# Performance work log

Measured on AMD Instinct MI355X. Metric: run time of the kernel, lower is better.

The kernel has to match this reference:

```python
import jax, jax.numpy as jnp
import numpy as np
from jax import lax

B, T, D, H = 64, 512, 256, 256


def lstm_scan(x_seq, Wih, Whh, bih, bhh):
    """Run an LSTMCell over time. x_seq: [B, T, D] -> hidden states [B, T, H].
    Gate order i, f, g, o (torch LSTMCell convention)."""
    Bv, Tv, _ = x_seq.shape
    Hv = Whh.shape[1]
    # Precompute input projection once: [B, T, 4H]
    x_proj = jnp.einsum('btd,gd->btg', x_seq, Wih) + bih + bhh

    def step(carry, xp):
        h, c = carry
        gates = xp + h @ Whh.T  # [B, 4H]
        i, f, g, o = jnp.split(gates, 4, axis=-1)
        c = jax.nn.sigmoid(f) * c + jax.nn.sigmoid(i) * jnp.tanh(g)
        h = jax.nn.sigmoid(o) * jnp.tanh(c)
        return (h, c), h

    init = (jnp.zeros((Bv, Hv), x_seq.dtype), jnp.zeros((Bv, Hv), x_seq.dtype))
    _, hs = lax.scan(step, init, jnp.swapaxes(x_proj, 0, 1))  # [T, B, H]
    return jnp.swapaxes(hs, 0, 1)


def bilstm(x, input_length, Wih_f, Whh_f, bih_f, bhh_f, Wih_b, Whh_b, bih_b, bhh_b):
    Bv, L, _ = x.shape
    t = jnp.arange(L)
    lens = input_length.astype(jnp.int32)
    # Inversed input exactly as _get_inversed_input: for t < len -> x[len-1-t],
    # for t >= len -> x[L-1-(t-len)] (unused tail, faithful to original).
    inv_idx = L - 1 - ((L - lens[:, None] + t[None, :]) % L)  # [B, L]
    xn = jnp.take_along_axis(x, inv_idx[:, :, None], axis=1)

    fwd_h = lstm_scan(x, Wih_f, Whh_f, bih_f, bhh_f)   # [B, L, H]
    bwd_h = lstm_scan(xn, Wih_b, Whh_b, bih_b, bhh_b)  # [B, L, H]

    # Re-reverse the backward states over valid region; zero-pad beyond length.
    mask = t[None, :] < lens[:, None]                   # [B, L]
    bwd_idx = jnp.clip(lens[:, None] - 1 - t[None, :], 0, L - 1)
    bwd_g = jnp.take_along_axis(bwd_h, bwd_idx[:, :, None], axis=1)
    out = jnp.concatenate([fwd_h, bwd_g], axis=-1)      # [B, L, 2H]
    return jnp.where(mask[:, :, None], out, jnp.zeros((), out.dtype))


def setup_inputs() -> dict:
    key = jax.random.key(0)
    ks = jax.random.split(key, 10)
    s = 0.05
    return {
        'x': jax.random.normal(ks[0], (B, T, D), jnp.float32),
        'input_length': jax.random.randint(ks[1], (B,), 1, T + 1, jnp.int32),
        'Wih_f': jax.random.normal(ks[2], (4 * H, D), jnp.float32) * s,
        'Whh_f': jax.random.normal(ks[3], (4 * H, H), jnp.float32) * s,
        'bih_f': jax.random.normal(ks[4], (4 * H,), jnp.float32) * s,
        'bhh_f': jax.random.normal(ks[5], (4 * H,), jnp.float32) * s,
        'Wih_b': jax.random.normal(ks[6], (4 * H, D), jnp.float32) * s,
        'Whh_b': jax.random.normal(ks[7], (4 * H, H), jnp.float32) * s,
        'bih_b': jax.random.normal(ks[8], (4 * H,), jnp.float32) * s,
        'bhh_b': jax.random.normal(ks[9], (4 * H,), jnp.float32) * s,
    }


def reference(x, input_length, Wih_f, Whh_f, bih_f, bhh_f, Wih_b, Whh_b, bih_b, bhh_b):
    return bilstm(x, input_length, Wih_f, Whh_f, bih_f, bhh_f, Wih_b, Whh_b, bih_b, bhh_b)
```

## Files before the change

### kernel.cpp

```cpp
#include <hip/hip_runtime.h>
#include <cstdio>


typedef unsigned short ushort_t;
typedef __attribute__((ext_vector_type(8))) short short8;
typedef __attribute__((ext_vector_type(4))) float f32x4;

__device__ __forceinline__ ushort_t f2bf(float f) {
    union { float f; unsigned u; } v; v.f = f;
    unsigned r = v.u + 0x7fffu + ((v.u >> 16) & 1u);
    return (ushort_t)(r >> 16);
}
__device__ __forceinline__ float bf2f(ushort_t h) {
    union { unsigned u; float f; } v; v.u = ((unsigned)h) << 16;
    return v.f;
}

__device__ __forceinline__ float fexp2(float x) {
#if __has_builtin(__builtin_amdgcn_exp2f)
    return __builtin_amdgcn_exp2f(x);
#else
    return exp2f(x);
#endif
}
__device__ __forceinline__ float frcp(float x) {
#if __has_builtin(__builtin_amdgcn_rcpf)
    return __builtin_amdgcn_rcpf(x);
#else
    return 1.0f / x;
#endif
}
__device__ __forceinline__ float fsig(float x) {
    return frcp(1.0f + fexp2(-1.44269504089f * x));
}
__device__ __forceinline__ float ftanh(float x) {
    float e = fexp2(2.88539008178f * x);
    return 1.0f - 2.0f * frcp(e + 1.0f);
}

__device__ __forceinline__ int dot4(int a, int b, int c) {
#if __has_builtin(__builtin_amdgcn_sdot4)
    return __builtin_amdgcn_sdot4(a, b, c, false);
#else
    int r = c;
    r += ((a << 24) >> 24) * ((b << 24) >> 24);
    r += ((a << 16) >> 24) * ((b << 16) >> 24);
    r += ((a << 8) >> 24) * ((b << 8) >> 24);
    r += (a >> 24) * (b >> 24);
    return r;
#endif
}

__device__ __forceinline__ void lds_barrier() {
    asm volatile("s_waitcnt lgkmcnt(0)\n\ts_barrier" ::: "memory");
}

__global__ __launch_bounds__(256) void k_f2bf(const float* __restrict__ in,
                                              ushort_t* __restrict__ out, int n) {
    int i = (blockIdx.x * 256 + threadIdx.x) * 4;
    if (i + 3 < n) {
        float4 v = *(const float4*)&in[i];
        ushort4 o;
        o.x = f2bf(v.x); o.y = f2bf(v.y); o.z = f2bf(v.z); o.w = f2bf(v.w);
        *(ushort4*)&out[i] = o;
    }
}

__global__ __launch_bounds__(256) void k_wih(const float* __restrict__ wihf,
                                             const float* __restrict__ wihb,
                                             ushort_t* __restrict__ dst) {
    int d = blockIdx.y;
    int n = blockIdx.x * 4 + (threadIdx.x >> 6);
    int l = threadIdx.x & 63;
    const float* src = (d ? wihb : wihf) + (size_t)n * 256;
    float4 v = *(const float4*)&src[l * 4];
    int np = (n & 255) * 4 + (n >> 8);
    ushort4 o;
    o.x = f2bf(v.x); o.y = f2bf(v.y); o.z = f2bf(v.z); o.w = f2bf(v.w);
    *(ushort4*)&dst[((size_t)d * 1024 + np) * 256 + l * 4] = o;
}

__global__ __launch_bounds__(256) void k_bias(const float* __restrict__ bihf,
                                              const float* __restrict__ bhhf,
                                              const float* __restrict__ bihb,
                                              const float* __restrict__ bhhb,
                                              float* __restrict__ bv) {
    int i = blockIdx.x * 256 + threadIdx.x;
    int d = i >> 10, n = i & 1023;
    float s = d ? (bihb[n] + bhhb[n]) : (bihf[n] + bhhf[n]);
    bv[d * 1024 + (n & 255) * 4 + (n >> 8)] = s;
}

__global__ __launch_bounds__(256) void k_quant(const float* __restrict__ whhf,
                                               const float* __restrict__ whhb,
                                               int* __restrict__ wq4,
                                               float* __restrict__ fscale4) {
    int rowg = blockIdx.x * 4 + (threadIdx.x >> 6);
    int l = threadIdx.x & 63;
    int d = rowg >> 10;
    int row = rowg & 1023;
    const float* W = (d ? whhb : whhf) + (size_t)row * 256;
    float4 v = *(const float4*)&W[l * 4];
    float m = fmaxf(fmaxf(fabsf(v.x), fabsf(v.y)), fmaxf(fabsf(v.z), fabsf(v.w)));
    #pragma unroll
    for (int off = 32; off > 0; off >>= 1) m = fmaxf(m, __shfl_xor(m, off));
    float inv = (m > 0.0f) ? (127.0f / m) : 0.0f;
    int q0 = __float2int_rn(v.x * inv);
    int q1 = __float2int_rn(v.y * inv);
    int q2 = __float2int_rn(v.z * inv);
    int q3 = __float2int_rn(v.w * inv);
    q0 = min(127, max(-127, q0)); q1 = min(127, max(-127, q1));
    q2 = min(127, max(-127, q2)); q3 = min(127, max(-127, q3));
    int packed = (q0 & 255) | ((q1 & 255) << 8) | ((q2 & 255) << 16) | ((q3 & 255) << 24);
    int j = row & 255, gate = row >> 8;
    wq4[d * 65536 + l * 1024 + j * 4 + gate] = packed;
    if (l == 0) fscale4[d * 1024 + j * 4 + gate] = m / (127.0f * 127.0f);
}

#define LDSOFF(r, kc) ((r) * 32 + ((((kc) + ((r) >> 1)) & 3) * 8))

__global__ __launch_bounds__(256) void k_gemm(const ushort_t* __restrict__ A,
                                              const ushort_t* __restrict__ Bw,
                                              const float* __restrict__ biasv,
                                              ushort_t* __restrict__ Xp) {
    const int dir = blockIdx.z;
    const ushort_t* Bmat = Bw + dir * 262144;
    const float* bv = biasv + dir * 1024;
    ushort_t* C = Xp + (size_t)dir * 33554432;
    const int tn = blockIdx.x;
    const int tm = blockIdx.y;
    const int tid = threadIdx.x;
    const int w = tid >> 6, l = tid & 63;
    const int wm = w & 1, wn = w >> 1;

    __shared__ ushort_t As[128 * 32];
    __shared__ ushort_t Bs[128 * 32];

    f32x4 acc[4][4];
    #pragma unroll
    for (int i = 0; i < 4; i++)
        #pragma unroll
        for (int jj = 0; jj < 4; jj++) acc[i][jj] = (f32x4){0.f, 0.f, 0.f, 0.f};

    const int r0 = tid >> 2, c0 = tid & 3;
    const int r1 = (tid + 256) >> 2, c1 = tid & 3;

    for (int kb = 0; kb < 8; kb++) {
        __syncthreads();
        {
            short8 a0 = *(const short8*)&A[((size_t)(tm * 128 + r0)) * 256 + kb * 32 + c0 * 8];
            short8 a1 = *(const short8*)&A[((size_t)(tm * 128 + r1)) * 256 + kb * 32 + c1 * 8];
            short8 b0 = *(const short8*)&Bmat[((size_t)(tn * 128 + r0)) * 256 + kb * 32 + c0 * 8];
            short8 b1 = *(const short8*)&Bmat[((size_t)(tn * 128 + r1)) * 256 + kb * 32 + c1 * 8];
            *(short8*)&As[LDSOFF(r0, c0)] = a0;
            *(short8*)&As[LDSOFF(r1, c1)] = a1;
            *(short8*)&Bs[LDSOFF(r0, c0)] = b0;
            *(short8*)&Bs[LDSOFF(r1, c1)] = b1;
        }
        __syncthreads();
        short8 af[4], bfr[4];
        const int q = l >> 4;
        #pragma unroll
        for (int mt = 0; mt < 4; mt++) {
            int rr = wm * 64 + mt * 16 + (l & 15);
            af[mt] = *(const short8*)&As[LDSOFF(rr, q)];
        }
        #pragma unroll
        for (int nt = 0; nt < 4; nt++) {
            int rr = wn * 64 + nt * 16 + (l & 15);
            bfr[nt] = *(const short8*)&Bs[LDSOFF(rr, q)];
        }
        #pragma unroll
        for (int mt = 0; mt < 4; mt++)
            #pragma unroll
            for (int nt = 0; nt < 4; nt++)
                acc[mt][nt] = __builtin_amdgcn_mfma_f32_16x16x32_bf16(
                    af[mt], bfr[nt], acc[mt][nt], 0, 0, 0);
    }
    #pragma unroll
    for (int nt = 0; nt < 4; nt++) {
        int n = tn * 128 + wn * 64 + nt * 16 + (l & 15);
        float bn = bv[n];
        #pragma unroll
        for (int mt = 0; mt < 4; mt++) {
            #pragma unroll
            for (int rr = 0; rr < 4; rr++) {
                int m = tm * 128 + wm * 64 + mt * 16 + (l >> 4) * 4 + rr;
                C[(size_t)m * 1024 + n] = f2bf(acc[mt][nt][rr] + bn);
            }
        }
    }
}

__device__ __forceinline__ int time_idx(int s, int len, int d) {
    int sc = (s < len - 1) ? s : (len - 1);
    return (d == 0) ? sc : (len - 1 - sc);
}

__global__ __launch_bounds__(512, 2) void k_rec(const ushort_t* __restrict__ xproj,
                                                const int* __restrict__ wq4,
                                                const float* __restrict__ fscale4,
                                                const int* __restrict__ lens,
                                                float* __restrict__ out) {
    const int b = blockIdx.x, d = blockIdx.y;
    const int tid = threadIdx.x;
    const int j = tid & 255, p = tid >> 8;
    int len = lens[b];
    if (len < 1) len = 1;
    if (len > 512) len = 512;
    const ushort_t* xp = xproj + ((size_t)d * 64 + b) * 524288;
    const int* wq = wq4 + d * 65536;
    float2 fr = *(const float2*)&fscale4[d * 1024 + j * 4 + p * 2];

    int wa[64], wb[64];
    #pragma unroll
    for (int kc = 0; kc < 64; kc++) {
        int2 v = *(const int2*)&wq[kc * 1024 + j * 4 + p * 2];
        wa[kc] = v.x; wb[kc] = v.y;
    }
    #pragma unroll
    for (int kc = 0; kc < 64; kc++) {
        asm volatile("" : "+v"(wa[kc]), "+v"(wb[kc]));
    }

    __shared__ int h8[2][64] __attribute__((aligned(16)));
    __shared__ float gA[256], oA[256];
    if (tid < 64) h8[0][tid] = 0;

    {
        float4 z = {0.f, 0.f, 0.f, 0.f};
        int total4 = (512 - len) * 64;
        for (int i = tid; i < total4; i += 512) {
            int t = len + (i >> 6);
            int c4 = i & 63;
            *(float4*)&out[((size_t)b * 512 + t) * 512 + d * 256 + c4 * 4] = z;
        }
    }
    __syncthreads();

    float c_state = 0.0f;
    unsigned xv0 = *(const unsigned*)&xp[(size_t)time_idx(0, len, d) * 1024 + j * 4 + p * 2];
    unsigned xv1 = *(const unsigned*)&xp[(size_t)time_idx(1, len, d) * 1024 + j * 4 + p * 2];

    for (int s = 0; s < len; s++) {
        unsigned xc = xv0;
        xv0 = xv1;
        unsigned xn = *(const unsigned*)&xp[(size_t)time_idx(s + 2, len, d) * 1024 + j * 4 + p * 2];

        const int4* hb = (const int4*)&h8[s & 1][0];
        int a0 = 0, c0 = 0, a1 = 0, c1 = 0;
        #pragma unroll
        for (int kc = 0; kc < 16; kc++) {
            int4 hv = hb[kc];
            a0 = dot4(wa[kc * 4 + 0], hv.x, a0); c0 = dot4(wa[kc * 4 + 1], hv.y, c0);
            a0 = dot4(wa[kc * 4 + 2], hv.z, a0); c0 = dot4(wa[kc * 4 + 3], hv.w, c0);
            a1 = dot4(wb[kc * 4 + 0], hv.x, a1); c1 = dot4(wb[kc * 4 + 1], hv.y, c1);
            a1 = dot4(wb[kc * 4 + 2], hv.z, a1); c1 = dot4(wb[kc * 4 + 3], hv.w, c1);
        }
        float pre0 = bf2f((ushort_t)(xc & 0xffffu)) + fr.x * (float)(a0 + c0);
        float pre1 = bf2f((ushort_t)(xc >> 16))     + fr.y * (float)(a1 + c1);

        if (p) {
            gA[j] = ftanh(pre0);
            oA[j] = fsig(pre1);
        }
        lds_barrier();
        if (!p) {
            float ig = fsig(pre0), fg = fsig(pre1);
            c_state = fg * c_state + ig * gA[j];
            float h = oA[j] * ftanh(c_state);
            int t = time_idx(s, len, d);
            out[((size_t)b * 512 + t) * 512 + d * 256 + j] = h;
            int q = __float2int_rn(h * 127.0f);
            q = min(127, max(-127, q));
            ((char*)&h8[1 - (s & 1)][0])[j] = (char)q;
        }
        xv1 = xn;
        lds_barrier();
    }
}

extern "C" void kernel_launch(void* const* d_in, const int* in_sizes, int n_in,
                              void* d_out, int out_size, void* d_ws, size_t ws_size,
                              hipStream_t stream) {
    (void)in_sizes; (void)n_in; (void)out_size;
    const float* x    = (const float*)d_in[0];
    const int*   lens = (const int*)d_in[1];
    const float* wihf = (const float*)d_in[2];
    const float* whhf = (const float*)d_in[3];
    const float* bihf = (const float*)d_in[4];
    const float* bhhf = (const float*)d_in[5];
    const float* wihb = (const float*)d_in[6];
    const float* whhb = (const float*)d_in[7];
    const float* bihb = (const float*)d_in[8];
    const float* bhhb = (const float*)d_in[9];
    float* out = (float*)d_out;

    char* ws = (char*)d_ws;
    ushort_t* xbf    = (ushort_t*)(ws + 0);
    ushort_t* wihbf  = (ushort_t*)(ws + 16777216);
    float*    biasv  = (float*)(ws + 17825792);
    int*      wq4    = (int*)(ws + 17833984);
    float*    fscale4= (float*)(ws + 18358272);
    ushort_t* xproj  = (ushort_t*)(ws + 18366464);
    const size_t REQ = 18366464 + 134217728ull;
    if (ws_size < REQ) {
        fprintf(stderr, "kernel_launch: ws too small: %zu < %zu\n", ws_size, REQ);
    }

    k_f2bf<<<8192, 256, 0, stream>>>(x, xbf, 8388608);
    k_wih<<<dim3(256, 2), 256, 0, stream>>>(wihf, wihb, wihbf);
    k_bias<<<8, 256, 0, stream>>>(bihf, bhhf, bihb, bhhb, biasv);
    k_quant<<<512, 256, 0, stream>>>(whhf, whhb, wq4, fscale4);
    k_gemm<<<dim3(8, 256, 2), 256, 0, stream>>>(xbf, wihbf, biasv, xproj);
    k_rec<<<dim3(64, 2), 512, 0, stream>>>(xproj, wq4, fscale4, lens, out);
}
```

Measured before the change: 640.4 us.

## Use int8 MFMA for recurrent matvec and compute all four gates per thread

Replaces the per-thread sdot4 loops in the recurrent kernel with int8 16x16x64 MFMA instructions. The quantized Whh is stored in an MFMA fragment layout, and h is broadcast across the N dimension. Each active lane now selects its row result and computes all four gates itself, which removes the gate exchange through shared memory and one barrier per step. In exchange, half the lanes idle during the gate math, and most of the MFMA N columns compute redundant results.

```diff
diff --git a/kernel.cpp b/kernel.cpp
--- a/kernel.cpp
+++ b/kernel.cpp
@@ -5,6 +5,7 @@
 typedef unsigned short ushort_t;
 typedef __attribute__((ext_vector_type(8))) short short8;
 typedef __attribute__((ext_vector_type(4))) float f32x4;
+typedef __attribute__((ext_vector_type(4))) int i32x4;
 
 __device__ __forceinline__ ushort_t f2bf(float f) {
     union { float f; unsigned u; } v; v.f = f;
@@ -36,19 +37,6 @@
 __device__ __forceinline__ float ftanh(float x) {
     float e = fexp2(2.88539008178f * x);
     return 1.0f - 2.0f * frcp(e + 1.0f);
-}
-
-__device__ __forceinline__ int dot4(int a, int b, int c) {
-#if __has_builtin(__builtin_amdgcn_sdot4)
-    return __builtin_amdgcn_sdot4(a, b, c, false);
-#else
-    int r = c;
-    r += ((a << 24) >> 24) * ((b << 24) >> 24);
-    r += ((a << 16) >> 24) * ((b << 16) >> 24);
-    r += ((a << 8) >> 24) * ((b << 8) >> 24);
-    r += (a >> 24) * (b >> 24);
-    return r;
-#endif
 }
 
 __device__ __forceinline__ void lds_barrier() {
@@ -93,7 +81,7 @@
 
 __global__ __launch_bounds__(256) void k_quant(const float* __restrict__ whhf,
                                                const float* __restrict__ whhb,
-                                               int* __restrict__ wq4,
+                                               int* __restrict__ wmf,
                                                float* __restrict__ fscale4) {
     int rowg = blockIdx.x * 4 + (threadIdx.x >> 6);
     int l = threadIdx.x & 63;
@@ -113,8 +101,11 @@
     q2 = min(127, max(-127, q2)); q3 = min(127, max(-127, q3));
     int packed = (q0 & 255) | ((q1 & 255) << 8) | ((q2 & 255) << 16) | ((q3 & 255) << 24);
     int j = row & 255, gate = row >> 8;
-    wq4[d * 65536 + l * 1024 + j * 4 + gate] = packed;
-    if (l == 0) fscale4[d * 1024 + j * 4 + gate] = m / (127.0f * 127.0f);
+    int row_p = j * 4 + gate;
+    int Mt = row_p >> 4, rl = row_p & 15;
+    int Kt = l >> 4, lg = (l >> 2) & 3, dw = l & 3;
+    wmf[d * 65536 + ((Mt * 4 + Kt) * 64 + lg * 16 + rl) * 4 + dw] = packed;
+    if (l == 0) fscale4[d * 1024 + row_p] = m / (127.0f * 127.0f);
 }
 
 #define LDSOFF(r, kc) ((r) * 32 + ((((kc) + ((r) >> 1)) & 3) * 8))
@@ -198,34 +189,40 @@
 }
 
 __global__ __launch_bounds__(512, 2) void k_rec(const ushort_t* __restrict__ xproj,
-                                                const int* __restrict__ wq4,
+                                                const int* __restrict__ wmf,
                                                 const float* __restrict__ fscale4,
                                                 const int* __restrict__ lens,
                                                 float* __restrict__ out) {
     const int b = blockIdx.x, d = blockIdx.y;
     const int tid = threadIdx.x;
-    const int j = tid & 255, p = tid >> 8;
+    const int w = tid >> 6, l = tid & 63;
     int len = lens[b];
     if (len < 1) len = 1;
     if (len > 512) len = 512;
     const ushort_t* xp = xproj + ((size_t)d * 64 + b) * 524288;
-    const int* wq = wq4 + d * 65536;
-    float2 fr = *(const float2*)&fscale4[d * 1024 + j * 4 + p * 2];
-
-    int wa[64], wb[64];
-    #pragma unroll
-    for (int kc = 0; kc < 64; kc++) {
-        int2 v = *(const int2*)&wq[kc * 1024 + j * 4 + p * 2];
-        wa[kc] = v.x; wb[kc] = v.y;
-    }
-    #pragma unroll
-    for (int kc = 0; kc < 64; kc++) {
-        asm volatile("" : "+v"(wa[kc]), "+v"(wb[kc]));
-    }
-
-    __shared__ int h8[2][64] __attribute__((aligned(16)));
-    __shared__ float gA[256], oA[256];
-    if (tid < 64) h8[0][tid] = 0;
+
+    const int rg = l >> 4;
+    const int til = l & 7;
+    const bool act = (l & 15) < 8;
+    const int j = (w * 8 + til) * 4 + rg;
+
+    i32x4 wf[8][4];
+    const int* wb = wmf + d * 65536;
+    #pragma unroll
+    for (int i = 0; i < 8; i++)
+        #pragma unroll
+        for (int kt = 0; kt < 4; kt++)
+            wf[i][kt] = *(const i32x4*)&wb[(((w * 8 + i) * 4 + kt) * 64 + l) * 4];
+    #pragma unroll
+    for (int i = 0; i < 8; i++)
+        #pragma unroll
+        for (int kt = 0; kt < 4; kt++)
+            asm volatile("" : "+v"(wf[i][kt]));
+
+    float4 fr = *(const float4*)&fscale4[d * 1024 + 4 * j];
+
+    __shared__ char h8[2][256] __attribute__((aligned(16)));
+    if (tid < 64) ((int*)h8)[tid] = 0;
 
     {
         float4 z = {0.f, 0.f, 0.f, 0.f};
@@ -239,41 +236,50 @@
     __syncthreads();
 
     float c_state = 0.0f;
-    unsigned xv0 = *(const unsigned*)&xp[(size_t)time_idx(0, len, d) * 1024 + j * 4 + p * 2];
-    unsigned xv1 = *(const unsigned*)&xp[(size_t)time_idx(1, len, d) * 1024 + j * 4 + p * 2];
+    uint2 xv0 = *(const uint2*)&xp[(size_t)time_idx(0, len, d) * 1024 + 4 * j];
+    uint2 xv1 = *(const uint2*)&xp[(size_t)time_idx(1, len, d) * 1024 + 4 * j];
+    const i32x4 z4 = {0, 0, 0, 0};
 
     for (int s = 0; s < len; s++) {
-        unsigned xc = xv0;
+        uint2 xc = xv0;
         xv0 = xv1;
-        unsigned xn = *(const unsigned*)&xp[(size_t)time_idx(s + 2, len, d) * 1024 + j * 4 + p * 2];
-
-        const int4* hb = (const int4*)&h8[s & 1][0];
-        int a0 = 0, c0 = 0, a1 = 0, c1 = 0;
-        #pragma unroll
-        for (int kc = 0; kc < 16; kc++) {
-            int4 hv = hb[kc];
-            a0 = dot4(wa[kc * 4 + 0], hv.x, a0); c0 = dot4(wa[kc * 4 + 1], hv.y, c0);
-            a0 = dot4(wa[kc * 4 + 2], hv.z, a0); c0 = dot4(wa[kc * 4 + 3], hv.w, c0);
-            a1 = dot4(wb[kc * 4 + 0], hv.x, a1); c1 = dot4(wb[kc * 4 + 1], hv.y, c1);
-            a1 = dot4(wb[kc * 4 + 2], hv.z, a1); c1 = dot4(wb[kc * 4 + 3], hv.w, c1);
-        }
-        float pre0 = bf2f((ushort_t)(xc & 0xffffu)) + fr.x * (float)(a0 + c0);
-        float pre1 = bf2f((ushort_t)(xc >> 16))     + fr.y * (float)(a1 + c1);
-
-        if (p) {
-            gA[j] = ftanh(pre0);
-            oA[j] = fsig(pre1);
-        }
-        lds_barrier();
-        if (!p) {
-            float ig = fsig(pre0), fg = fsig(pre1);
-            c_state = fg * c_state + ig * gA[j];
-            float h = oA[j] * ftanh(c_state);
+        uint2 xn = *(const uint2*)&xp[(size_t)time_idx(s + 2, len, d) * 1024 + 4 * j];
+
+        const char* hb = h8[s & 1];
+        i32x4 h0 = *(const i32x4*)(hb + rg * 16);
+        i32x4 h1 = *(const i32x4*)(hb + 64 + rg * 16);
+        i32x4 h2 = *(const i32x4*)(hb + 128 + rg * 16);
+        i32x4 h3 = *(const i32x4*)(hb + 192 + rg * 16);
+
+        i32x4 acc[8];
+        #pragma unroll
+        for (int i = 0; i < 8; i++) {
+            i32x4 a = __builtin_amdgcn_mfma_i32_16x16x64_i8(wf[i][0], h0, z4, 0, 0, 0);
+            a = __builtin_amdgcn_mfma_i32_16x16x64_i8(wf[i][1], h1, a, 0, 0, 0);
+            a = __builtin_amdgcn_mfma_i32_16x16x64_i8(wf[i][2], h2, a, 0, 0, 0);
+            acc[i] = __builtin_amdgcn_mfma_i32_16x16x64_i8(wf[i][3], h3, a, 0, 0, 0);
+        }
+
+        if (act) {
+            i32x4 q0 = (til & 1) ? acc[1] : acc[0];
+            i32x4 q1 = (til & 1) ? acc[3] : acc[2];
+            i32x4 q2 = (til & 1) ? acc[5] : acc[4];
+            i32x4 q3 = (til & 1) ? acc[7] : acc[6];
+            i32x4 r0 = (til & 2) ? q1 : q0;
+            i32x4 r1 = (til & 2) ? q3 : q2;
+            i32x4 u  = (til & 4) ? r1 : r0;
+            float pi = bf2f((ushort_t)(xc.x & 0xffffu)) + fr.x * (float)u.x;
+            float pf = bf2f((ushort_t)(xc.x >> 16))     + fr.y * (float)u.y;
+            float pg = bf2f((ushort_t)(xc.y & 0xffffu)) + fr.z * (float)u.z;
+            float po = bf2f((ushort_t)(xc.y >> 16))     + fr.w * (float)u.w;
+            float ig = fsig(pi), fg = fsig(pf), gg = ftanh(pg), og = fsig(po);
+            c_state = fg * c_state + ig * gg;
+            float h = og * ftanh(c_state);
             int t = time_idx(s, len, d);
             out[((size_t)b * 512 + t) * 512 + d * 256 + j] = h;
             int q = __float2int_rn(h * 127.0f);
             q = min(127, max(-127, q));
-            ((char*)&h8[1 - (s & 1)][0])[j] = (char)q;
+            h8[1 - (s & 1)][j] = (char)q;
         }
         xv1 = xn;
         lds_barrier();
@@ -300,7 +306,7 @@
     ushort_t* xbf    = (ushort_t*)(ws + 0);
     ushort_t* wihbf  = (ushort_t*)(ws + 16777216);
     float*    biasv  = (float*)(ws + 17825792);
-    int*      wq4    = (int*)(ws + 17833984);
+    int*      wmf    = (int*)(ws + 17833984);
     float*    fscale4= (float*)(ws + 18358272);
     ushort_t* xproj  = (ushort_t*)(ws + 18366464);
     const size_t REQ = 18366464 + 134217728ull;
@@ -311,7 +317,7 @@
     k_f2bf<<<8192, 256, 0, stream>>>(x, xbf, 8388608);
     k_wih<<<dim3(256, 2), 256, 0, stream>>>(wihf, wihb, wihbf);
     k_bias<<<8, 256, 0, stream>>>(bihf, bhhf, bihb, bhhb, biasv);
-    k_quant<<<512, 256, 0, stream>>>(whhf, whhb, wq4, fscale4);
+    k_quant<<<512, 256, 0, stream>>>(whhf, whhb, wmf, fscale4);
     k_gemm<<<dim3(8, 256, 2), 256, 0, stream>>>(xbf, wihbf, biasv, xproj);
-    k_rec<<<dim3(64, 2), 512, 0, stream>>>(xproj, wq4, fscale4, lens, out);
-}
+    k_rec<<<dim3(64, 2), 512, 0, stream>>>(xproj, wmf, fscale4, lens, out);
+}
```

New measurement: 562.2 us. 1.14x faster.
